# Optimization experiments

Hardware: AMD Instinct MI355X
Metric: run time of the kernel (lower is better)

Reference implementation:

```python
import jax, jax.numpy as jnp
import numpy as np

B, N, IN_DIM, H, D = 4, 2048, 128, 4, 64
NEG_SLOPE = 0.2
MASK_VAL = -1e9


def setup_inputs() -> dict:
    key = jax.random.key(0)
    k1, k2, k3, k4, k5 = jax.random.split(key, 5)
    x = jax.random.normal(k1, (B, N, IN_DIM), dtype=jnp.float32)
    adj = jax.random.randint(k2, (N, N), 0, 2, dtype=jnp.int32)
    W = jax.random.normal(k3, (H * D, IN_DIM), dtype=jnp.float32) * 0.05
    att_src = jax.random.normal(k4, (1, H, D), dtype=jnp.float32) * 0.05
    att_dst = jax.random.normal(k5, (1, H, D), dtype=jnp.float32) * 0.05
    return {"x": x, "adj": adj, "W": W, "att_src": att_src, "att_dst": att_dst}


def reference(x, adj, W, att_src, att_dst):
    # linear (no bias), torch layout: y = x @ W.T  -> [B,N,H*D]
    h = jnp.einsum('bni,oi->bno', x, W).reshape(B, N, H, D).transpose(0, 2, 1, 3)  # [B,H,N,D]
    e_src = jnp.einsum('bhnd,hd->bhn', h, att_src[0])  # [B,H,N]
    e_dst = jnp.einsum('bhnd,hd->bhn', h, att_dst[0])  # [B,H,N]
    # additive score: e[b,h,i,j] = leaky_relu(e_src[b,h,i] + e_dst[b,h,j])
    e = jax.nn.leaky_relu(e_src[..., :, None] + e_dst[..., None, :], NEG_SLOPE)  # [B,H,N,N]
    e = jnp.where(adj[None, None] <= 0, MASK_VAL, e)
    attn = jax.nn.softmax(e, axis=-1)  # dropout inactive (inference)
    out = jnp.einsum('bhij,bhjd->bhid', attn, h)  # [B,H,N,D]
    return out.transpose(0, 2, 1, 3).reshape(B, N, H * D)  # concat heads
```

## Files before the change

### kernel.cpp

```cpp
#include <hip/hip_runtime.h>


#define NDIM 2048
#define NEG_SLOPE 0.2f
#define LOG2E 1.4426950408889634f

typedef __bf16 bf16x8 __attribute__((ext_vector_type(8)));
typedef __bf16 bf16x4 __attribute__((ext_vector_type(4)));
typedef float  f32x4  __attribute__((ext_vector_type(4)));

#define LP 136

__device__ static inline void load_lds16(const void* g, void* l) {
    __builtin_amdgcn_global_load_lds(
        (const __attribute__((address_space(1))) unsigned*)g,
        (__attribute__((address_space(3))) unsigned*)l, 16, 0, 0);
}

__global__ __launch_bounds__(256) void adj_pack(const int* __restrict__ adj,
                                                unsigned* __restrict__ bits) {
    const int t = threadIdx.x;
    const int q = blockIdx.x * 256 + t;
    int4 a = ((const int4*)adj)[q];
    unsigned nib = (unsigned)(a.x > 0) | ((unsigned)(a.y > 0) << 1) |
                   ((unsigned)(a.z > 0) << 2) | ((unsigned)(a.w > 0) << 3);
    unsigned v = nib << ((t & 7) * 4);
    v |= __shfl_xor(v, 1, 64);
    v |= __shfl_xor(v, 2, 64);
    v |= __shfl_xor(v, 4, 64);
    if ((t & 7) == 0) bits[q >> 3] = v;
}

__global__ __launch_bounds__(256) void gat_linear(
    const float* __restrict__ x, const float* __restrict__ W,
    const float* __restrict__ att_src, const float* __restrict__ att_dst,
    __bf16* __restrict__ h_t, float* __restrict__ es_ws, float* __restrict__ ed_ws)
{
    const int t    = threadIdx.x;
    const int head = blockIdx.x & 3;
    const int n0g  = (blockIdx.x >> 2) * 64;
    const int b    = n0g >> 11;
    const int n0   = n0g & (NDIM - 1);
    const int bh   = b * 4 + head;

    __shared__ __align__(16) __bf16 Wl[64][LP];
    __shared__ __align__(16) __bf16 Xl[64][LP];

    #pragma unroll
    for (int i = 0; i < 8; ++i) {
        int idx = t + i * 256;
        int r = idx >> 5, c4 = idx & 31;
        float4 wv = *((const float4*)(W + (size_t)(head * 64 + r) * 128) + c4);
        bf16x4 bv;
        bv[0] = (__bf16)wv.x; bv[1] = (__bf16)wv.y; bv[2] = (__bf16)wv.z; bv[3] = (__bf16)wv.w;
        *(bf16x4*)&Wl[r][c4 * 4] = bv;
    }
    #pragma unroll
    for (int i = 0; i < 8; ++i) {
        int idx = t + i * 256;
        int r = idx >> 5, c4 = idx & 31;
        float4 xv = *((const float4*)(x + (size_t)(n0g + r) * 128) + c4);
        bf16x4 bv;
        bv[0] = (__bf16)xv.x; bv[1] = (__bf16)xv.y; bv[2] = (__bf16)xv.z; bv[3] = (__bf16)xv.w;
        *(bf16x4*)&Xl[r][c4 * 4] = bv;
    }
    __syncthreads();

    const int lane = t & 63, w = t >> 6;
    const int m = lane & 15, q4 = lane >> 4;

    bf16x8 bfr[4];
    #pragma unroll
    for (int ks = 0; ks < 4; ++ks)
        bfr[ks] = *(const bf16x8*)&Xl[w * 16 + m][ks * 32 + q4 * 8];

    f32x4 acc[4];
    #pragma unroll
    for (int c = 0; c < 4; ++c) acc[c] = (f32x4){0.f, 0.f, 0.f, 0.f};

    #pragma unroll
    for (int ct = 0; ct < 4; ++ct) {
        #pragma unroll
        for (int ks = 0; ks < 4; ++ks) {
            bf16x8 afr = *(const bf16x8*)&Wl[ct * 16 + m][ks * 32 + q4 * 8];
            acc[ct] = __builtin_amdgcn_mfma_f32_16x16x32_bf16(afr, bfr[ks], acc[ct], 0, 0, 0);
        }
    }

    const int nloc = n0 + w * 16 + m;
    float esA = 0.f, edA = 0.f;
    #pragma unroll
    for (int ct = 0; ct < 4; ++ct) {
        float4 aS = *(const float4*)(att_src + head * 64 + ct * 16 + q4 * 4);
        float4 aD = *(const float4*)(att_dst + head * 64 + ct * 16 + q4 * 4);
        #pragma unroll
        for (int r = 0; r < 4; ++r) {
            float v = acc[ct][r];
            int   d = ct * 16 + q4 * 4 + r;
            h_t[(size_t)(bh * 64 + d) * NDIM + nloc] = (__bf16)v;
            esA += v * ((const float*)&aS)[r];
            edA += v * ((const float*)&aD)[r];
        }
    }
    esA += __shfl_xor(esA, 16, 64); esA += __shfl_xor(esA, 32, 64);
    edA += __shfl_xor(edA, 16, 64); edA += __shfl_xor(edA, 32, 64);
    if (lane < 16) {
        es_ws[bh * NDIM + nloc] = esA * LOG2E;
        ed_ws[bh * NDIM + nloc] = edA * LOG2E;
    }
}

__global__ __launch_bounds__(256) void gat_attn(
    const unsigned long long* __restrict__ bits, const __bf16* __restrict__ h_t,
    const float* __restrict__ es_ws, const float* __restrict__ ed_ws,
    float* __restrict__ out)
{
    const int blk = blockIdx.x;
    const int bh  = blk & 15;
    const int i0  = (blk >> 4) * 64;
    const int t   = threadIdx.x;
    const int lane = t & 63, w = t >> 6;
    const int m = lane & 15, q4 = lane >> 4;

    __shared__ __align__(16) __bf16 Hl[2][64][64];

    const int r0 = w * 16 + (lane >> 3);
    const int r1 = r0 + 8;
    const int c8 = lane & 7;
    const __bf16* g0 = h_t + ((size_t)(bh * 64 + r0)) * NDIM + ((c8 ^ (r0 & 7)) * 8);
    const __bf16* g1 = h_t + ((size_t)(bh * 64 + r1)) * NDIM + ((c8 ^ (r1 & 7)) * 8);
    __bf16* l0a = &Hl[0][r0][c8 * 8];
    __bf16* l0b = &Hl[0][r1][c8 * 8];
    __bf16* l1a = &Hl[1][r0][c8 * 8];
    __bf16* l1b = &Hl[1][r1][c8 * 8];

    const float es2 = es_ws[bh * NDIM + i0 + w * 16 + m];
    const unsigned long long* brow = bits + (size_t)(i0 + w * 16 + m) * 32;
    const float* edp = ed_ws + bh * NDIM + q4 * 8;

    load_lds16(g0, l0a);
    load_lds16(g1, l0b);
    float eb[2][16];
    unsigned long long bwb[2];
    #pragma unroll
    for (int g = 0; g < 4; ++g)
        *(float4*)&eb[0][g * 4] = *(const float4*)(edp + (g >> 1) * 32 + (g & 1) * 4);
    bwb[0] = brow[0];

    f32x4 acc[4], accl;
    #pragma unroll
    for (int c = 0; c < 4; ++c) acc[c] = (f32x4){0.f, 0.f, 0.f, 0.f};
    accl = (f32x4){0.f, 0.f, 0.f, 0.f};
    bf16x8 ones;
    #pragma unroll
    for (int jj = 0; jj < 8; ++jj) ones[jj] = (__bf16)1.0f;
    const int sw = m & 7;

    __syncthreads();

#define STEP(ITJ, P)                                                            \
    {                                                                           \
        const int itj = (ITJ);                                                  \
        if (itj < 31) {                                                         \
            load_lds16(g0 + (itj + 1) * 64, (P) ? l0a : l1a);                   \
            load_lds16(g1 + (itj + 1) * 64, (P) ? l0b : l1b);                   \
            const float* ep = edp + (itj + 1) * 64;                             \
            _Pragma("unroll")                                                   \
            for (int g = 0; g < 4; ++g)                                         \
                *(float4*)&eb[(P) ^ 1][g * 4] =                                 \
                    *(const float4*)(ep + (g >> 1) * 32 + (g & 1) * 4);         \
            bwb[(P) ^ 1] = brow[itj + 1];                                       \
        }                                                                       \
        bf16x8 af[2];                                                           \
        _Pragma("unroll")                                                       \
        for (int ks = 0; ks < 2; ++ks) {                                        \
            unsigned bm = (unsigned)(bwb[P] >> (ks * 32 + q4 * 8)) & 0xFFu;     \
            _Pragma("unroll")                                                   \
            for (int jj = 0; jj < 8; ++jj) {                                    \
                float s = es2 + eb[P][ks * 8 + jj];                             \
                s = fmaxf(s, NEG_SLOPE * s);                                    \
                s = ((bm >> jj) & 1u) ? s : -10000.0f;                          \
                af[ks][jj] = (__bf16)__builtin_amdgcn_exp2f(s);                 \
            }                                                                   \
        }                                                                       \
        _Pragma("unroll")                                                       \
        for (int ks = 0; ks < 2; ++ks) {                                        \
            accl = __builtin_amdgcn_mfma_f32_16x16x32_bf16(af[ks], ones, accl, 0, 0, 0); \
            _Pragma("unroll")                                                   \
            for (int ct = 0; ct < 4; ++ct) {                                    \
                bf16x8 bfr = *(const bf16x8*)&Hl[P][ct * 16 + m][(((ks * 4 + q4) ^ sw)) * 8]; \
                acc[ct] = __builtin_amdgcn_mfma_f32_16x16x32_bf16(af[ks], bfr, acc[ct], 0, 0, 0); \
            }                                                                   \
        }                                                                       \
        __syncthreads();                                                        \
    }

    for (int it2 = 0; it2 < 16; ++it2) {
        STEP(it2 * 2, 0);
        STEP(it2 * 2 + 1, 1);
    }
#undef STEP

    float invr[4];
    #pragma unroll
    for (int r = 0; r < 4; ++r) invr[r] = 1.f / accl[r];

    const int b = bh >> 2, head = bh & 3;
    float* ob = out + ((size_t)(b * NDIM + i0 + w * 16)) * 256 + head * 64;
    #pragma unroll
    for (int ct = 0; ct < 4; ++ct) {
        #pragma unroll
        for (int r = 0; r < 4; ++r) {
            ob[(size_t)(q4 * 4 + r) * 256 + ct * 16 + m] = acc[ct][r] * invr[r];
        }
    }
}

extern "C" void kernel_launch(void* const* d_in, const int* in_sizes, int n_in,
                              void* d_out, int out_size, void* d_ws, size_t ws_size,
                              hipStream_t stream) {
    const float* x       = (const float*)d_in[0];
    const int*   adj     = (const int*)d_in[1];
    const float* W       = (const float*)d_in[2];
    const float* att_src = (const float*)d_in[3];
    const float* att_dst = (const float*)d_in[4];
    float* out = (float*)d_out;

    __bf16*   h_t   = (__bf16*)d_ws;
    float*    es_ws = (float*)((char*)d_ws + (size_t)4 * 1024 * 1024);
    float*    ed_ws = es_ws + 16 * NDIM;
    unsigned* bitsp = (unsigned*)(ed_ws + 16 * NDIM);

    adj_pack<<<NDIM * NDIM / 4 / 256, 256, 0, stream>>>(adj, bitsp);
    gat_linear<<<512, 256, 0, stream>>>(x, W, att_src, att_dst, h_t, es_ws, ed_ws);
    gat_attn<<<512, 256, 0, stream>>>((const unsigned long long*)bitsp, h_t, es_ws, ed_ws, out);
}
```

Before: 109.1 us.

## Factor exp of leaky-relu score into precomputed exponentials and widen LDS tiles

Uses exp2(lrelu(a+b)) = max(2^a·2^b, 2^(0.2a)·2^(0.2b)) so that per-node exponentials are computed once in the linear kernel. The inner loop then needs only two multiplies, a max and a bitmask AND per score, with no transcendental per pair. The H tile in shared memory is also doubled to 128 columns, which halves the number of barriers and loads. The risks are overflow or underflow of the unnormalised exponentials, since there is no max subtraction, and twice the LDS and ed bandwidth.

After: 111.0 us. Within noise of the previous version (+1.8%).

```diff
diff --git a/kernel.cpp b/kernel.cpp
--- a/kernel.cpp
+++ b/kernel.cpp
@@ -2,7 +2,6 @@
 
 
 #define NDIM 2048
-#define NEG_SLOPE 0.2f
 #define LOG2E 1.4426950408889634f
 
 typedef __bf16 bf16x8 __attribute__((ext_vector_type(8)));
@@ -105,8 +104,14 @@
     esA += __shfl_xor(esA, 16, 64); esA += __shfl_xor(esA, 32, 64);
     edA += __shfl_xor(edA, 16, 64); edA += __shfl_xor(edA, 32, 64);
     if (lane < 16) {
-        es_ws[bh * NDIM + nloc] = esA * LOG2E;
-        ed_ws[bh * NDIM + nloc] = edA * LOG2E;
+        float s2 = esA * LOG2E, d2 = edA * LOG2E;
+        float2 ev, dv;
+        ev.x = __builtin_amdgcn_exp2f(s2);
+        ev.y = __builtin_amdgcn_exp2f(0.2f * s2);
+        dv.x = __builtin_amdgcn_exp2f(d2);
+        dv.y = __builtin_amdgcn_exp2f(0.2f * d2);
+        ((float2*)es_ws)[(size_t)bh * NDIM + nloc] = ev;
+        ((float2*)ed_ws)[(size_t)bh * NDIM + nloc] = dv;
     }
 }
 
@@ -122,29 +127,34 @@
     const int lane = t & 63, w = t >> 6;
     const int m = lane & 15, q4 = lane >> 4;
 
-    __shared__ __align__(16) __bf16 Hl[2][64][64];
-
-    const int r0 = w * 16 + (lane >> 3);
-    const int r1 = r0 + 8;
-    const int c8 = lane & 7;
-    const __bf16* g0 = h_t + ((size_t)(bh * 64 + r0)) * NDIM + ((c8 ^ (r0 & 7)) * 8);
-    const __bf16* g1 = h_t + ((size_t)(bh * 64 + r1)) * NDIM + ((c8 ^ (r1 & 7)) * 8);
-    __bf16* l0a = &Hl[0][r0][c8 * 8];
-    __bf16* l0b = &Hl[0][r1][c8 * 8];
-    __bf16* l1a = &Hl[1][r0][c8 * 8];
-    __bf16* l1b = &Hl[1][r1][c8 * 8];
-
-    const float es2 = es_ws[bh * NDIM + i0 + w * 16 + m];
+    __shared__ __align__(16) __bf16 Hl[2][64][128];
+
+    const int lh   = lane >> 4;
+    const int c8   = lane & 7;
+    const int half = (lane >> 3) & 1;
+    const __bf16* gA  = h_t + (size_t)(bh * 64 + w * 16 + lh) * NDIM
+                        + half * 64 + (c8 ^ lh) * 8;
+    const __bf16* gB  = h_t + (size_t)(bh * 64 + w * 16 + 4 + lh) * NDIM
+                        + half * 64 + ((c8 ^ lh ^ 4)) * 8;
+    const __bf16* gA2 = gA + 8 * NDIM;
+    const __bf16* gB2 = gB + 8 * NDIM;
+    __bf16* const ld0 = &Hl[0][0][0] + w * 2048 + lane * 8;
+
+    const float2 eg = ((const float2*)es_ws)[(size_t)bh * NDIM + i0 + w * 16 + m];
+    const float egx = eg.x, egy = eg.y;
     const unsigned long long* brow = bits + (size_t)(i0 + w * 16 + m) * 32;
-    const float* edp = ed_ws + bh * NDIM + q4 * 8;
-
-    load_lds16(g0, l0a);
-    load_lds16(g1, l0b);
-    float eb[2][16];
+    const float* edp = ed_ws + ((size_t)bh * NDIM + q4 * 8) * 2;
+
+    load_lds16(gA,  ld0);
+    load_lds16(gB,  ld0 + 512);
+    load_lds16(gA2, ld0 + 1024);
+    load_lds16(gB2, ld0 + 1536);
+
+    float fh[2][32];
     unsigned long long bwb[2];
     #pragma unroll
-    for (int g = 0; g < 4; ++g)
-        *(float4*)&eb[0][g * 4] = *(const float4*)(edp + (g >> 1) * 32 + (g & 1) * 4);
+    for (int g = 0; g < 8; ++g)
+        *(float4*)&fh[0][g * 4] = *(const float4*)(edp + (g >> 2) * 64 + (g & 3) * 4);
     bwb[0] = brow[0];
 
     f32x4 acc[4], accl;
@@ -158,46 +168,55 @@
 
     __syncthreads();
 
-#define STEP(ITJ, P)                                                            \
-    {                                                                           \
-        const int itj = (ITJ);                                                  \
-        if (itj < 31) {                                                         \
-            load_lds16(g0 + (itj + 1) * 64, (P) ? l0a : l1a);                   \
-            load_lds16(g1 + (itj + 1) * 64, (P) ? l0b : l1b);                   \
-            const float* ep = edp + (itj + 1) * 64;                             \
-            _Pragma("unroll")                                                   \
-            for (int g = 0; g < 4; ++g)                                         \
-                *(float4*)&eb[(P) ^ 1][g * 4] =                                 \
-                    *(const float4*)(ep + (g >> 1) * 32 + (g & 1) * 4);         \
-            bwb[(P) ^ 1] = brow[itj + 1];                                       \
-        }                                                                       \
-        bf16x8 af[2];                                                           \
-        _Pragma("unroll")                                                       \
-        for (int ks = 0; ks < 2; ++ks) {                                        \
-            unsigned bm = (unsigned)(bwb[P] >> (ks * 32 + q4 * 8)) & 0xFFu;     \
-            _Pragma("unroll")                                                   \
-            for (int jj = 0; jj < 8; ++jj) {                                    \
-                float s = es2 + eb[P][ks * 8 + jj];                             \
-                s = fmaxf(s, NEG_SLOPE * s);                                    \
-                s = ((bm >> jj) & 1u) ? s : -10000.0f;                          \
-                af[ks][jj] = (__bf16)__builtin_amdgcn_exp2f(s);                 \
-            }                                                                   \
-        }                                                                       \
-        _Pragma("unroll")                                                       \
-        for (int ks = 0; ks < 2; ++ks) {                                        \
+#define STEP(ITJ, FP, HB)                                                        \
+    {                                                                            \
+        const int itj = (ITJ);                                                   \
+        if (itj < 31) {                                                          \
+            const float* ep = edp + (size_t)(itj + 1) * 128;                     \
+            _Pragma("unroll")                                                    \
+            for (int g = 0; g < 8; ++g)                                          \
+                *(float4*)&fh[(FP) ^ 1][g * 4] =                                 \
+                    *(const float4*)(ep + (g >> 2) * 64 + (g & 3) * 4);          \
+            bwb[(FP) ^ 1] = brow[itj + 1];                                       \
+        }                                                                        \
+        bf16x8 af[2];                                                            \
+        _Pragma("unroll")                                                        \
+        for (int ks = 0; ks < 2; ++ks) {                                         \
+            unsigned bm = (unsigned)(bwb[FP] >> (ks * 32 + q4 * 8)) & 0xFFu;     \
+            _Pragma("unroll")                                                    \
+            for (int jj = 0; jj < 8; ++jj) {                                     \
+                float t1 = egx * fh[FP][ks * 16 + jj * 2];                       \
+                float t2 = egy * fh[FP][ks * 16 + jj * 2 + 1];                   \
+                float p = fmaxf(t1, t2);                                         \
+                int mk = ((int)(bm << (31 - jj))) >> 31;                         \
+                p = __int_as_float(__float_as_int(p) & mk);                      \
+                af[ks][jj] = (__bf16)p;                                          \
+            }                                                                    \
+        }                                                                        \
+        _Pragma("unroll")                                                        \
+        for (int ks = 0; ks < 2; ++ks) {                                         \
             accl = __builtin_amdgcn_mfma_f32_16x16x32_bf16(af[ks], ones, accl, 0, 0, 0); \
-            _Pragma("unroll")                                                   \
-            for (int ct = 0; ct < 4; ++ct) {                                    \
-                bf16x8 bfr = *(const bf16x8*)&Hl[P][ct * 16 + m][(((ks * 4 + q4) ^ sw)) * 8]; \
+            _Pragma("unroll")                                                    \
+            for (int ct = 0; ct < 4; ++ct) {                                     \
+                bf16x8 bfr = *(const bf16x8*)&Hl[HB][ct * 16 + m][(FP) * 64 + ((ks * 4 + q4) ^ sw) * 8]; \
                 acc[ct] = __builtin_amdgcn_mfma_f32_16x16x32_bf16(af[ks], bfr, acc[ct], 0, 0, 0); \
-            }                                                                   \
-        }                                                                       \
-        __syncthreads();                                                        \
-    }
-
-    for (int it2 = 0; it2 < 16; ++it2) {
-        STEP(it2 * 2, 0);
-        STEP(it2 * 2 + 1, 1);
+            }                                                                    \
+        }                                                                        \
+    }
+
+    for (int ph = 0; ph < 16; ++ph) {
+        const int Pb = ph & 1;
+        if (ph < 15) {
+            const size_t tb = (size_t)(ph + 1) * 128;
+            __bf16* dst = ld0 + (Pb ^ 1) * 8192;
+            load_lds16(gA  + tb, dst);
+            load_lds16(gB  + tb, dst + 512);
+            load_lds16(gA2 + tb, dst + 1024);
+            load_lds16(gB2 + tb, dst + 1536);
+        }
+        STEP(2 * ph,     0, Pb)
+        STEP(2 * ph + 1, 1, Pb)
+        __syncthreads();
     }
 #undef STEP
 
@@ -228,8 +247,8 @@
 
     __bf16*   h_t   = (__bf16*)d_ws;
     float*    es_ws = (float*)((char*)d_ws + (size_t)4 * 1024 * 1024);
-    float*    ed_ws = es_ws + 16 * NDIM;
-    unsigned* bitsp = (unsigned*)(ed_ws + 16 * NDIM);
+    float*    ed_ws = es_ws + (size_t)16 * NDIM * 2;
+    unsigned* bitsp = (unsigned*)(ed_ws + (size_t)16 * NDIM * 2);
 
     adj_pack<<<NDIM * NDIM / 4 / 256, 256, 0, stream>>>(adj, bitsp);
     gat_linear<<<512, 256, 0, stream>>>(x, W, att_src, att_dst, h_t, es_ws, ed_ws);
```

## Merge pre-kernels and split attention key range across two wave groups

Applied to the files above, without the earlier changes.

Merges the adjacency bit-packing and linear projection kernels into one launch, with extra blocks doing the packing, which saves one kernel launch and lets the two jobs overlap. The attention kernel now uses 512 threads per block: two groups of four waves each handle half of the key dimension, and the partial accumulators are reduced through LDS before normalisation. This doubles the waves resident per output tile and halves the serial loop length, since only 512 blocks exist for a large GPU. In exchange it adds an LDS reduction, an extra barrier and twice the LDS footprint per block.

New measurement: 106.3 us (median of 2 runs). 2.6% less time.

```diff
diff --git a/kernel.cpp b/kernel.cpp
--- a/kernel.cpp
+++ b/kernel.cpp
@@ -17,26 +17,28 @@
         (__attribute__((address_space(3))) unsigned*)l, 16, 0, 0);
 }
 
-__global__ __launch_bounds__(256) void adj_pack(const int* __restrict__ adj,
-                                                unsigned* __restrict__ bits) {
+__global__ __launch_bounds__(256) void gat_pre(
+    const float* __restrict__ x, const int* __restrict__ adj,
+    const float* __restrict__ W, const float* __restrict__ att_src,
+    const float* __restrict__ att_dst, __bf16* __restrict__ h_t,
+    float* __restrict__ es_ws, float* __restrict__ ed_ws,
+    unsigned* __restrict__ bits)
+{
     const int t = threadIdx.x;
-    const int q = blockIdx.x * 256 + t;
-    int4 a = ((const int4*)adj)[q];
-    unsigned nib = (unsigned)(a.x > 0) | ((unsigned)(a.y > 0) << 1) |
-                   ((unsigned)(a.z > 0) << 2) | ((unsigned)(a.w > 0) << 3);
-    unsigned v = nib << ((t & 7) * 4);
-    v |= __shfl_xor(v, 1, 64);
-    v |= __shfl_xor(v, 2, 64);
-    v |= __shfl_xor(v, 4, 64);
-    if ((t & 7) == 0) bits[q >> 3] = v;
-}
-
-__global__ __launch_bounds__(256) void gat_linear(
-    const float* __restrict__ x, const float* __restrict__ W,
-    const float* __restrict__ att_src, const float* __restrict__ att_dst,
-    __bf16* __restrict__ h_t, float* __restrict__ es_ws, float* __restrict__ ed_ws)
-{
-    const int t    = threadIdx.x;
+
+    if (blockIdx.x >= 512) {
+        const int q = (blockIdx.x - 512) * 256 + t;
+        int4 a = ((const int4*)adj)[q];
+        unsigned nib = (unsigned)(a.x > 0) | ((unsigned)(a.y > 0) << 1) |
+                       ((unsigned)(a.z > 0) << 2) | ((unsigned)(a.w > 0) << 3);
+        unsigned v = nib << ((t & 7) * 4);
+        v |= __shfl_xor(v, 1, 64);
+        v |= __shfl_xor(v, 2, 64);
+        v |= __shfl_xor(v, 4, 64);
+        if ((t & 7) == 0) bits[q >> 3] = v;
+        return;
+    }
+
     const int head = blockIdx.x & 3;
     const int n0g  = (blockIdx.x >> 2) * 64;
     const int b    = n0g >> 11;
@@ -110,7 +112,7 @@
     }
 }
 
-__global__ __launch_bounds__(256) void gat_attn(
+__global__ __launch_bounds__(512, 4) void gat_attn(
     const unsigned long long* __restrict__ bits, const __bf16* __restrict__ h_t,
     const float* __restrict__ es_ws, const float* __restrict__ ed_ws,
     float* __restrict__ out)
@@ -120,31 +122,33 @@
     const int i0  = (blk >> 4) * 64;
     const int t   = threadIdx.x;
     const int lane = t & 63, w = t >> 6;
+    const int gJ = w >> 2, wl = w & 3;
     const int m = lane & 15, q4 = lane >> 4;
 
-    __shared__ __align__(16) __bf16 Hl[2][64][64];
-
-    const int r0 = w * 16 + (lane >> 3);
+    __shared__ __align__(16) __bf16 Hl[2][2][64][64];
+
+    const int r0 = wl * 16 + (lane >> 3);
     const int r1 = r0 + 8;
     const int c8 = lane & 7;
-    const __bf16* g0 = h_t + ((size_t)(bh * 64 + r0)) * NDIM + ((c8 ^ (r0 & 7)) * 8);
-    const __bf16* g1 = h_t + ((size_t)(bh * 64 + r1)) * NDIM + ((c8 ^ (r1 & 7)) * 8);
-    __bf16* l0a = &Hl[0][r0][c8 * 8];
-    __bf16* l0b = &Hl[0][r1][c8 * 8];
-    __bf16* l1a = &Hl[1][r0][c8 * 8];
-    __bf16* l1b = &Hl[1][r1][c8 * 8];
-
-    const float es2 = es_ws[bh * NDIM + i0 + w * 16 + m];
-    const unsigned long long* brow = bits + (size_t)(i0 + w * 16 + m) * 32;
-    const float* edp = ed_ws + bh * NDIM + q4 * 8;
+    const size_t jbase = (size_t)gJ * 1024;
+    const __bf16* g0 = h_t + ((size_t)(bh * 64 + r0)) * NDIM + jbase + ((c8 ^ (r0 & 7)) * 8);
+    const __bf16* g1 = h_t + ((size_t)(bh * 64 + r1)) * NDIM + jbase + ((c8 ^ (r1 & 7)) * 8);
+    __bf16* l0a = &Hl[gJ][0][r0][c8 * 8];
+    __bf16* l0b = &Hl[gJ][0][r1][c8 * 8];
+    __bf16* l1a = &Hl[gJ][1][r0][c8 * 8];
+    __bf16* l1b = &Hl[gJ][1][r1][c8 * 8];
+
+    const float es2 = es_ws[bh * NDIM + i0 + wl * 16 + m];
+    const unsigned long long* brow = bits + (size_t)(i0 + wl * 16 + m) * 32 + gJ * 16;
+    const float* edp = ed_ws + bh * NDIM + jbase + q4 * 8;
 
     load_lds16(g0, l0a);
     load_lds16(g1, l0b);
     float eb[2][16];
     unsigned long long bwb[2];
     #pragma unroll
-    for (int g = 0; g < 4; ++g)
-        *(float4*)&eb[0][g * 4] = *(const float4*)(edp + (g >> 1) * 32 + (g & 1) * 4);
+    for (int g4 = 0; g4 < 4; ++g4)
+        *(float4*)&eb[0][g4 * 4] = *(const float4*)(edp + (g4 >> 1) * 32 + (g4 & 1) * 4);
     bwb[0] = brow[0];
 
     f32x4 acc[4], accl;
@@ -161,14 +165,14 @@
 #define STEP(ITJ, P)                                                            \
     {                                                                           \
         const int itj = (ITJ);                                                  \
-        if (itj < 31) {                                                         \
+        if (itj < 15) {                                                         \
             load_lds16(g0 + (itj + 1) * 64, (P) ? l0a : l1a);                   \
             load_lds16(g1 + (itj + 1) * 64, (P) ? l0b : l1b);                   \
             const float* ep = edp + (itj + 1) * 64;                             \
             _Pragma("unroll")                                                   \
-            for (int g = 0; g < 4; ++g)                                         \
-                *(float4*)&eb[(P) ^ 1][g * 4] =                                 \
-                    *(const float4*)(ep + (g >> 1) * 32 + (g & 1) * 4);         \
+            for (int g4 = 0; g4 < 4; ++g4)                                      \
+                *(float4*)&eb[(P) ^ 1][g4 * 4] =                                \
+                    *(const float4*)(ep + (g4 >> 1) * 32 + (g4 & 1) * 4);       \
             bwb[(P) ^ 1] = brow[itj + 1];                                       \
         }                                                                       \
         bf16x8 af[2];                                                           \
@@ -188,30 +192,48 @@
             accl = __builtin_amdgcn_mfma_f32_16x16x32_bf16(af[ks], ones, accl, 0, 0, 0); \
             _Pragma("unroll")                                                   \
             for (int ct = 0; ct < 4; ++ct) {                                    \
-                bf16x8 bfr = *(const bf16x8*)&Hl[P][ct * 16 + m][(((ks * 4 + q4) ^ sw)) * 8]; \
+                bf16x8 bfr = *(const bf16x8*)&Hl[gJ][P][ct * 16 + m][((ks * 4 + q4) ^ sw) * 8]; \
                 acc[ct] = __builtin_amdgcn_mfma_f32_16x16x32_bf16(af[ks], bfr, acc[ct], 0, 0, 0); \
             }                                                                   \
         }                                                                       \
         __syncthreads();                                                        \
     }
 
-    for (int it2 = 0; it2 < 16; ++it2) {
+    for (int it2 = 0; it2 < 8; ++it2) {
         STEP(it2 * 2, 0);
         STEP(it2 * 2 + 1, 1);
     }
 #undef STEP
 
-    float invr[4];
-    #pragma unroll
-    for (int r = 0; r < 4; ++r) invr[r] = 1.f / accl[r];
-
-    const int b = bh >> 2, head = bh & 3;
-    float* ob = out + ((size_t)(b * NDIM + i0 + w * 16)) * 256 + head * 64;
-    #pragma unroll
-    for (int ct = 0; ct < 4; ++ct) {
-        #pragma unroll
-        for (int r = 0; r < 4; ++r) {
-            ob[(size_t)(q4 * 4 + r) * 256 + ct * 16 + m] = acc[ct][r] * invr[r];
+    float* sc = (float*)&Hl[0][0][0][0];
+    const int sidx = (wl * 64 + lane) * 24;
+    if (w >= 4) {
+        #pragma unroll
+        for (int ct = 0; ct < 4; ++ct) *(f32x4*)&sc[sidx + ct * 4] = acc[ct];
+        *(f32x4*)&sc[sidx + 16] = accl;
+    }
+    __syncthreads();
+    if (w < 4) {
+        #pragma unroll
+        for (int ct = 0; ct < 4; ++ct) {
+            f32x4 o = *(const f32x4*)&sc[sidx + ct * 4];
+            acc[ct] = acc[ct] + o;
+        }
+        f32x4 lo = *(const f32x4*)&sc[sidx + 16];
+        accl = accl + lo;
+
+        float invr[4];
+        #pragma unroll
+        for (int r = 0; r < 4; ++r) invr[r] = 1.f / accl[r];
+
+        const int b = bh >> 2, head = bh & 3;
+        float* ob = out + ((size_t)(b * NDIM + i0 + wl * 16)) * 256 + head * 64;
+        #pragma unroll
+        for (int ct = 0; ct < 4; ++ct) {
+            #pragma unroll
+            for (int r = 0; r < 4; ++r) {
+                ob[(size_t)(q4 * 4 + r) * 256 + ct * 16 + m] = acc[ct][r] * invr[r];
+            }
         }
     }
 }
@@ -231,7 +253,6 @@
     float*    ed_ws = es_ws + 16 * NDIM;
     unsigned* bitsp = (unsigned*)(ed_ws + 16 * NDIM);
 
-    adj_pack<<<NDIM * NDIM / 4 / 256, 256, 0, stream>>>(adj, bitsp);
-    gat_linear<<<512, 256, 0, stream>>>(x, W, att_src, att_dst, h_t, es_ws, ed_ws);
-    gat_attn<<<512, 256, 0, stream>>>((const unsigned long long*)bitsp, h_t, es_ws, ed_ws, out);
-}
+    gat_pre<<<4608, 256, 0, stream>>>(x, adj, W, att_src, att_dst, h_t, es_ws, ed_ws, bitsp);
+    gat_attn<<<512, 512, 0, stream>>>((const unsigned long long*)bitsp, h_t, es_ws, ed_ws, out);
+}
```
